# Kernel tuning notes

Hardware: AMD Instinct MI355X
Metric: run time of the kernel (lower is better)

## Reference

```python
import jax, jax.numpy as jnp
import numpy as np

D = 1024          # dim_in == dim_out
H = 16            # num_heads
G = 4             # num_kv_groups
HD = D // H       # head_dim = 64
GS = H // G       # group_size = 4
S = 2048          # context_length / seq_len
B = 2
EPS = 1e-05


def setup_inputs() -> dict:
    key = jax.random.key(0)
    ks = jax.random.split(key, 12)
    sd = 0.02
    return {
        "x":  jax.random.normal(ks[0], (B, S, D), jnp.float32),
        # torch.nn.Linear weights are stored [out_features, in_features]
        "wq": jax.random.normal(ks[1], (D, D), jnp.float32) * sd,
        "wk": jax.random.normal(ks[2], (G * HD, D), jnp.float32) * sd,
        "wv": jax.random.normal(ks[3], (G * HD, D), jnp.float32) * sd,
        "wo": jax.random.normal(ks[4], (D, D), jnp.float32) * sd,
        "w1": jax.random.normal(ks[5], (4 * D, D), jnp.float32) * sd,
        "w2": jax.random.normal(ks[6], (D, 4 * D), jnp.float32) * sd,
        "g1": jnp.ones((D,), jnp.float32),
        "b1": jnp.zeros((D,), jnp.float32),
        "g2": jnp.ones((D,), jnp.float32),
        "b2": jnp.zeros((D,), jnp.float32),
    }


def _layernorm(x, gamma, beta):
    mean = jnp.mean(x, axis=-1, keepdims=True)
    var = jnp.var(x, axis=-1, keepdims=True)  # unbiased=False
    return (x - mean) * jax.lax.rsqrt(var + EPS) * gamma + beta


def _gelu_tanh(x):
    c = jnp.sqrt(jnp.asarray(2.0 / jnp.pi, x.dtype))
    return 0.5 * x * (1.0 + jnp.tanh(c * (x + 0.044715 * x ** 3)))


def _gqa(x, wq, wk, wv, wo):
    b, s, _ = x.shape
    q = (x @ wq.T).reshape(b, s, H, HD).transpose(0, 2, 1, 3)   # [B,H,S,hd]
    k = (x @ wk.T).reshape(b, s, G, HD).transpose(0, 2, 1, 3)   # [B,G,S,hd]
    v = (x @ wv.T).reshape(b, s, G, HD).transpose(0, 2, 1, 3)
    k = jnp.repeat(k, GS, axis=1)                               # [B,H,S,hd]
    v = jnp.repeat(v, GS, axis=1)
    scores = jnp.einsum('bhqd,bhkd->bhqk', q, k)                # [B,H,S,S]
    causal = jnp.tril(jnp.ones((s, s), bool))
    scores = jnp.where(causal, scores, -jnp.inf)
    attn = jax.nn.softmax(scores / jnp.sqrt(jnp.asarray(HD, scores.dtype)), axis=-1)
    ctx = jnp.einsum('bhqk,bhkd->bhqd', attn, v)                # [B,H,S,hd]
    ctx = ctx.transpose(0, 2, 1, 3).reshape(b, s, D)
    return ctx @ wo.T


def reference(x, wq, wk, wv, wo, w1, w2, g1, b1, g2, b2):
    h = x + _gqa(_layernorm(x, g1, b1), wq, wk, wv, wo)
    ff = _layernorm(h, g2, b2) @ w1.T
    ff = _gelu_tanh(ff) @ w2.T
    return h + ff
```

## Files before the change

kernel.cpp:

```cpp
#include <hip/hip_runtime.h>
#include <stdint.h>

typedef __bf16 bf16_t;
typedef bf16_t bf16x8 __attribute__((ext_vector_type(8)));
typedef bf16_t bf16x4 __attribute__((ext_vector_type(4)));
typedef float f32x4 __attribute__((ext_vector_type(4)));

#define DEVFN static __device__ __forceinline__

DEVFN void gload_lds16(const void* g, void* l) {
  __builtin_amdgcn_global_load_lds((const __attribute__((address_space(1))) void*)g,
                                   (__attribute__((address_space(3))) void*)l, 16, 0, 0);
}

DEVFN float gelu_f(float x) {
  float u = 0.7978845608028654f * (x + 0.044715f * x * x * x);
  float e = __expf(2.0f * u);
  float t = 1.0f - 2.0f / (e + 1.0f);
  return 0.5f * x * (1.0f + t);
}

template <int CTRL>
DEVFN float dpp_rot(float x) {
  int i = __builtin_bit_cast(int, x);
  int r = __builtin_amdgcn_update_dpp(i, i, CTRL, 0xF, 0xF, false);
  return __builtin_bit_cast(float, r);
}
DEVFN float dpp_sum16(float x) {
  x += dpp_rot<0x121>(x);
  x += dpp_rot<0x122>(x);
  x += dpp_rot<0x124>(x);
  x += dpp_rot<0x128>(x);
  return x;
}

__global__ void cvt_kernel(const float* __restrict__ s, bf16_t* __restrict__ d, int n4) {
  int i = blockIdx.x * blockDim.x + threadIdx.x;
  int stride = gridDim.x * blockDim.x;
  for (; i < n4; i += stride) {
    float4 v = ((const float4*)s)[i];
    bf16x4 o;
    o[0] = (bf16_t)v.x; o[1] = (bf16_t)v.y; o[2] = (bf16_t)v.z; o[3] = (bf16_t)v.w;
    ((bf16x4*)d)[i] = o;
  }
}

__global__ __launch_bounds__(256) void ln_kernel(const float* __restrict__ in,
                                                 const float* __restrict__ gamma,
                                                 const float* __restrict__ beta,
                                                 bf16_t* __restrict__ out) {
  const int row = blockIdx.x;
  const int tid = threadIdx.x;
  const float4 v = ((const float4*)(in + (size_t)row * 1024))[tid];
  float s = v.x + v.y + v.z + v.w;
  float q = v.x * v.x + v.y * v.y + v.z * v.z + v.w * v.w;
#pragma unroll
  for (int off = 1; off < 64; off <<= 1) {
    s += __shfl_xor(s, off);
    q += __shfl_xor(q, off);
  }
  __shared__ float ss[4], qs[4];
  if ((tid & 63) == 0) { ss[tid >> 6] = s; qs[tid >> 6] = q; }
  __syncthreads();
  s = ss[0] + ss[1] + ss[2] + ss[3];
  q = qs[0] + qs[1] + qs[2] + qs[3];
  const float mean = s * (1.0f / 1024.0f);
  const float var = q * (1.0f / 1024.0f) - mean * mean;
  const float rstd = rsqrtf(var + 1e-5f);
  const float4 g4 = ((const float4*)gamma)[tid];
  const float4 b4 = ((const float4*)beta)[tid];
  bf16x4 o;
  o[0] = (bf16_t)((v.x - mean) * rstd * g4.x + b4.x);
  o[1] = (bf16_t)((v.y - mean) * rstd * g4.y + b4.y);
  o[2] = (bf16_t)((v.z - mean) * rstd * g4.z + b4.z);
  o[3] = (bf16_t)((v.w - mean) * rstd * g4.w + b4.w);
  *(bf16x4*)(out + (size_t)row * 1024 + tid * 4) = o;
}

template <int EPI, int BM>
__global__ __launch_bounds__(256, (BM == 64 ? 4 : 2))
void gemm_bt(const bf16_t* __restrict__ A, const bf16_t* __restrict__ W,
             bf16_t* outb, float* outf, const float* resid, int M, int N, int K) {
  constexpr int MI = BM / 32;
  constexpr int WRS = BM / 2;
  __shared__ __align__(16) bf16_t As[BM * 32];
  __shared__ __align__(16) bf16_t Bs[128 * 32];
  const int tid = threadIdx.x;
  const int lane = tid & 63;
  const int wid = tid >> 6;
  const int l15 = lane & 15;
  const int l4 = lane >> 4;
  const int m0 = blockIdx.y * BM;
  const int n0 = blockIdx.x * 128;
  const int wr = wid >> 1;
  const int wc = wid & 1;

  const int sr = lane >> 2;
  const int sk = (lane & 3) * 8;
  const bf16_t* aBase;
  bf16_t* aDst0;
  if constexpr (BM == 128) {
    aBase = A + (size_t)(m0 + wid * 32 + sr) * K + sk;
    aDst0 = &As[wid * 1024];
  } else {
    aBase = A + (size_t)(m0 + wid * 16 + sr) * K + sk;
    aDst0 = &As[wid * 512];
  }
  const bf16_t* bBase = W + (size_t)(n0 + wid * 32 + sr) * K + sk;
  bf16_t* bDst0 = &Bs[wid * 1024];
  const size_t rowOff16 = (size_t)16 * K;

  f32x4 acc[MI][4] = {};

  for (int kt = 0; kt < K; kt += 32) {
    gload_lds16(aBase + kt, aDst0);
    if constexpr (BM == 128) gload_lds16(aBase + kt + rowOff16, aDst0 + 512);
    gload_lds16(bBase + kt, bDst0);
    gload_lds16(bBase + kt + rowOff16, bDst0 + 512);
    __syncthreads();
    bf16x8 af[MI], bfr[4];
#pragma unroll
    for (int i = 0; i < MI; ++i)
      af[i] = *(const bf16x8*)&As[(wr * WRS + i * 16 + l15) * 32 + l4 * 8];
#pragma unroll
    for (int j = 0; j < 4; ++j)
      bfr[j] = *(const bf16x8*)&Bs[(wc * 64 + j * 16 + l15) * 32 + l4 * 8];
#pragma unroll
    for (int i = 0; i < MI; ++i)
#pragma unroll
      for (int j = 0; j < 4; ++j)
        acc[i][j] = __builtin_amdgcn_mfma_f32_16x16x32_bf16(af[i], bfr[j], acc[i][j], 0, 0, 0);
    __syncthreads();
  }

  const int col0 = n0 + wc * 64 + l15;
  const int row0 = m0 + wr * WRS + l4 * 4;
#pragma unroll
  for (int i = 0; i < MI; ++i) {
#pragma unroll
    for (int r = 0; r < 4; ++r) {
      const size_t row = (size_t)(row0 + i * 16 + r);
#pragma unroll
      for (int j = 0; j < 4; ++j) {
        const size_t idx = row * N + col0 + j * 16;
        const float v = acc[i][j][r];
        if constexpr (EPI == 0) {
          outb[idx] = (bf16_t)v;
        } else if constexpr (EPI == 1) {
          outb[idx] = (bf16_t)gelu_f(v);
        } else {
          outf[idx] = resid[idx] + v;
        }
      }
    }
  }
}

static __device__ const int kQbTab[40] = {0,1,2,3,4,4,5,5,6,6,7,7,8,8,8,9,9,9,10,10,10,
                                          11,11,11,12,12,12,12,13,13,13,13,14,14,14,14,15,15,15,15};
static __device__ const int kCTab[40]  = {0,0,0,0,0,1,0,1,0,1,0,1,0,1,2,0,1,2,0,1,2,
                                          0,1,2,0,1,2,3,0,1,2,3,0,1,2,3,0,1,2,3};
static __device__ const int kPrefix16[16] = {0,1,2,3,4,6,8,10,12,15,18,21,24,28,32,36};

__global__ __launch_bounds__(256, 3) void attn_kernel(const bf16_t* __restrict__ qkv,
                                                      bf16_t* __restrict__ pO,
                                                      float* __restrict__ pML) {
  __shared__ __align__(16) bf16_t Ks[2][64 * 68];
  __shared__ __align__(16) bf16_t Vt[2][64 * 68];
  __shared__ __align__(16) bf16_t Ps[4][32 * 68];
  const int tid = threadIdx.x, lane = tid & 63, wid = tid >> 6;
  const int l15 = lane & 15, l4 = lane >> 4;
  const int bx = blockIdx.x;
  const int qb = kQbTab[bx] * 128;
  const int kv_lo = kCTab[bx] * 512;
  const int kv_hi = min(qb + 128, kv_lo + 512);
  const int h = blockIdx.y, b = blockIdx.z;
  const int g = h >> 2;
  const int slot = (b * 16 + h) * 40 + bx;
  const size_t RS = 1536;
  const bf16_t* qbase = qkv + (size_t)b * 2048 * RS + h * 64;
  const bf16_t* kbase = qkv + (size_t)b * 2048 * RS + 1024 + g * 64;
  const bf16_t* vbase = kbase + 256;
  const float C2S = 0.125f * 1.44269504088896340736f;

  bf16x8 qf[2][2];
#pragma unroll
  for (int rf = 0; rf < 2; ++rf)
#pragma unroll
    for (int kc = 0; kc < 2; ++kc) {
      bf16x8 raw = *(const bf16x8*)(qbase + (size_t)(qb + wid * 32 + rf * 16 + l15) * RS +
                                    kc * 32 + l4 * 8);
#pragma unroll
      for (int e = 0; e < 8; ++e) qf[rf][kc][e] = (bf16_t)((float)raw[e] * C2S);
    }

  f32x4 po[2][4] = {};
  float l_i[2][4] = {};

  const int sKrow = tid >> 2, sKc = (tid & 3) * 16;
  const int sVkey = tid & 63, sVd = (tid >> 6) * 16;
  const bf16_t* kRowPtr = kbase + (size_t)sKrow * RS + sKc;
  const bf16_t* vRowPtr = vbase + (size_t)sVkey * RS + sVd;

  uint4 k0 = *(const uint4*)(kRowPtr + (size_t)kv_lo * RS);
  uint4 k1 = *(const uint4*)(kRowPtr + (size_t)kv_lo * RS + 8);
  bf16x8 v0 = *(const bf16x8*)(vRowPtr + (size_t)kv_lo * RS);
  bf16x8 v1 = *(const bf16x8*)(vRowPtr + (size_t)kv_lo * RS + 8);
  *(uint4*)&Ks[0][sKrow * 68 + sKc] = k0;
  *(uint4*)&Ks[0][sKrow * 68 + sKc + 8] = k1;
#pragma unroll
  for (int i = 0; i < 8; ++i) {
    Vt[0][(sVd + i) * 68 + sVkey] = v0[i];
    Vt[0][(sVd + 8 + i) * 68 + sVkey] = v1[i];
  }

  const int fb0 = qb + wid * 32;
  int cur = 0;
  for (int kv0 = kv_lo; kv0 < kv_hi; kv0 += 64) {
    __syncthreads();
    const bool more = (kv0 + 64) < kv_hi;
    if (more) {
      const bf16_t* kp = kRowPtr + (size_t)(kv0 + 64) * RS;
      const bf16_t* vp = vRowPtr + (size_t)(kv0 + 64) * RS;
      k0 = *(const uint4*)kp;
      k1 = *(const uint4*)(kp + 8);
      v0 = *(const bf16x8*)vp;
      v1 = *(const bf16x8*)(vp + 8);
    }

    f32x4 sAcc[2][4] = {};
#pragma unroll
    for (int jt = 0; jt < 4; ++jt) {
#pragma unroll
      for (int kc = 0; kc < 2; ++kc) {
        bf16x8 kf = *(const bf16x8*)&Ks[cur][(jt * 16 + l15) * 68 + kc * 32 + l4 * 8];
        sAcc[0][jt] = __builtin_amdgcn_mfma_f32_16x16x32_bf16(qf[0][kc], kf, sAcc[0][jt], 0, 0, 0);
        sAcc[1][jt] = __builtin_amdgcn_mfma_f32_16x16x32_bf16(qf[1][kc], kf, sAcc[1][jt], 0, 0, 0);
      }
    }

#pragma unroll
    for (int rf = 0; rf < 2; ++rf) {
      const int fb = fb0 + rf * 16;
      if (kv0 > fb + 15) continue;
      bf16_t* psb = &Ps[wid][(rf * 16 + l4 * 4) * 68 + l15];
      float rsum[4] = {0.f, 0.f, 0.f, 0.f};
      const bool diag = (kv0 + 63 > fb);
#pragma unroll
      for (int jt = 0; jt < 4; ++jt)
#pragma unroll
        for (int r = 0; r < 4; ++r) {
          float sv = sAcc[rf][jt][r];
          if (diag) {
            const int key = kv0 + jt * 16 + l15;
            sv = (key <= fb + l4 * 4 + r) ? sv : -3.0e38f;
          }
          const float e = exp2f(sv);
          rsum[r] += e;
          psb[r * 68 + jt * 16] = (bf16_t)e;
        }
#pragma unroll
      for (int r = 0; r < 4; ++r) l_i[rf][r] += dpp_sum16(rsum[r]);
    }

    if (kv0 <= fb0 + 31) {
      const bool do0 = (kv0 <= fb0 + 15);
#pragma unroll
      for (int kc = 0; kc < 2; ++kc) {
        bf16x8 pa1 = *(const bf16x8*)&Ps[wid][(16 + l15) * 68 + kc * 32 + l4 * 8];
        bf16x8 pa0;
        if (do0) pa0 = *(const bf16x8*)&Ps[wid][l15 * 68 + kc * 32 + l4 * 8];
#pragma unroll
        for (int jd = 0; jd < 4; ++jd) {
          bf16x8 vf = *(const bf16x8*)&Vt[cur][(jd * 16 + l15) * 68 + kc * 32 + l4 * 8];
          if (do0) po[0][jd] = __builtin_amdgcn_mfma_f32_16x16x32_bf16(pa0, vf, po[0][jd], 0, 0, 0);
          po[1][jd] = __builtin_amdgcn_mfma_f32_16x16x32_bf16(pa1, vf, po[1][jd], 0, 0, 0);
        }
      }
    }

    if (more) {
      *(uint4*)&Ks[cur ^ 1][sKrow * 68 + sKc] = k0;
      *(uint4*)&Ks[cur ^ 1][sKrow * 68 + sKc + 8] = k1;
#pragma unroll
      for (int i = 0; i < 8; ++i) {
        Vt[cur ^ 1][(sVd + i) * 68 + sVkey] = v0[i];
        Vt[cur ^ 1][(sVd + 8 + i) * 68 + sVkey] = v1[i];
      }
    }
    cur ^= 1;
  }

#pragma unroll
  for (int rf = 0; rf < 2; ++rf) {
#pragma unroll
    for (int r = 0; r < 4; ++r) {
      const int lrow = wid * 32 + rf * 16 + l4 * 4 + r;
      if (l15 == 0) {
        pML[((size_t)slot * 128 + lrow) * 2] = 0.0f;
        pML[((size_t)slot * 128 + lrow) * 2 + 1] = l_i[rf][r];
      }
#pragma unroll
      for (int jd = 0; jd < 4; ++jd)
        pO[((size_t)slot * 128 + lrow) * 64 + jd * 16 + l15] = (bf16_t)po[rf][jd][r];
    }
  }
}

__global__ __launch_bounds__(256) void attn_combine(const bf16_t* __restrict__ pO,
                                                    const float* __restrict__ pML,
                                                    bf16_t* __restrict__ ctx) {
  const int i = blockIdx.x, h = blockIdx.y, b = blockIdx.z;
  const int C = (i >> 2) + 1;
  const int base = (b * 16 + h) * 40 + kPrefix16[i];
  const int row = threadIdx.x >> 1;
  const int half = (threadIdx.x & 1) * 32;
  float m = -3.0e38f;
  for (int c = 0; c < C; ++c)
    m = fmaxf(m, pML[((size_t)(base + c) * 128 + row) * 2]);
  float L = 0.0f, acc[32];
#pragma unroll
  for (int e = 0; e < 32; ++e) acc[e] = 0.0f;
  for (int c = 0; c < C; ++c) {
    const float mc = pML[((size_t)(base + c) * 128 + row) * 2];
    const float lc = pML[((size_t)(base + c) * 128 + row) * 2 + 1];
    const float w = exp2f(mc - m);
    L += w * lc;
    const bf16_t* op = pO + ((size_t)(base + c) * 128 + row) * 64 + half;
#pragma unroll
    for (int j = 0; j < 4; ++j) {
      bf16x8 v = *(const bf16x8*)(op + j * 8);
#pragma unroll
      for (int e = 0; e < 8; ++e) acc[j * 8 + e] += w * (float)v[e];
    }
  }
  const float inv = 1.0f / L;
  bf16_t* outp = ctx + ((size_t)b * 2048 + i * 128 + row) * 1024 + h * 64 + half;
#pragma unroll
  for (int j = 0; j < 4; ++j) {
    bf16x8 o;
#pragma unroll
    for (int e = 0; e < 8; ++e) o[e] = (bf16_t)(acc[j * 8 + e] * inv);
    *(bf16x8*)(outp + j * 8) = o;
  }
}

extern "C" void kernel_launch(void* const* d_in, const int* in_sizes, int n_in,
                              void* d_out, int out_size, void* d_ws, size_t ws_size,
                              hipStream_t stream) {
  const float* x = (const float*)d_in[0];
  const float* wq = (const float*)d_in[1];
  const float* wk = (const float*)d_in[2];
  const float* wv = (const float*)d_in[3];
  const float* wo = (const float*)d_in[4];
  const float* w1 = (const float*)d_in[5];
  const float* w2 = (const float*)d_in[6];
  const float* g1 = (const float*)d_in[7];
  const float* b1 = (const float*)d_in[8];
  const float* g2 = (const float*)d_in[9];
  const float* b2 = (const float*)d_in[10];
  float* out = (float*)d_out;

  char* ws = (char*)d_ws;
  bf16_t* qkv = (bf16_t*)(ws + 0);
  bf16_t* ctx = (bf16_t*)(ws + 12582912);
  bf16_t* wo_b = (bf16_t*)(ws + 20971520);
  bf16_t* wqkv_b = (bf16_t*)(ws + 23068672);
  bf16_t* h1 = (bf16_t*)(ws + 26214400);
  bf16_t* pO = (bf16_t*)(ws + 23068672);
  float* pML = (float*)(ws + 45088768);
  bf16_t* w1_b = (bf16_t*)(ws + 0);
  bf16_t* w2_b = (bf16_t*)(ws + 8388608);
  bf16_t* h2 = (bf16_t*)(ws + 16777216);
  bf16_t* ff = (bf16_t*)(ws + 25165824);

  auto cvt = [&](const float* s, bf16_t* d, int n) {
    int n4 = n / 4;
    int grid = (n4 + 255) / 256;
    if (grid > 2048) grid = 2048;
    cvt_kernel<<<grid, 256, 0, stream>>>(s, d, n4);
  };
  cvt(wq, wqkv_b, 1048576);
  cvt(wk, wqkv_b + 1048576, 262144);
  cvt(wv, wqkv_b + 1310720, 262144);
  cvt(wo, wo_b, 1048576);

  ln_kernel<<<4096, 256, 0, stream>>>(x, g1, b1, h1);
  gemm_bt<0, 64><<<dim3(12, 64), 256, 0, stream>>>(h1, wqkv_b, qkv, nullptr, nullptr, 4096, 1536, 1024);
  attn_kernel<<<dim3(40, 16, 2), 256, 0, stream>>>(qkv, pO, pML);
  cvt(w1, w1_b, 4194304);
  attn_combine<<<dim3(16, 16, 2), 256, 0, stream>>>(pO, pML, ctx);
  gemm_bt<2, 64><<<dim3(8, 64), 256, 0, stream>>>(ctx, wo_b, nullptr, out, x, 4096, 1024, 1024);
  cvt(w2, w2_b, 4194304);
  ln_kernel<<<4096, 256, 0, stream>>>(out, g2, b2, h2);
  gemm_bt<1, 128><<<dim3(32, 32), 256, 0, stream>>>(h2, w1_b, ff, nullptr, nullptr, 4096, 4096, 1024);
  gemm_bt<2, 64><<<dim3(8, 64), 256, 0, stream>>>(ff, w2_b, nullptr, out, out, 4096, 1024, 4096);
}
```

Before: 270.4 us.

## Double-buffer GEMM K-loop with 64-wide stages and merge weight conversion launches

The GEMM main loop now uses two LDS buffers, each holding two 32-wide K slices. The next 64-wide K stage is issued as async global-to-LDS loads before the current stage is computed, which halves the barrier count and overlaps memory with MFMA work. The min-blocks occupancy hint for BM=64 drops from 4 to 3 to allow for the larger LDS footprint. The four separate weight-conversion launches are also merged into one kernel to cut launch overhead. One risk: there is a single barrier per iteration while the next stage writes into the other buffer. Reads of that buffer from two iterations earlier are fenced only by that one barrier, which looks correct, but the async LDS writes are not explicitly waited on (vmcnt) before the barrier.

```diff
diff --git a/kernel.cpp b/kernel.cpp
--- a/kernel.cpp
+++ b/kernel.cpp
@@ -42,6 +42,26 @@
     bf16x4 o;
     o[0] = (bf16_t)v.x; o[1] = (bf16_t)v.y; o[2] = (bf16_t)v.z; o[3] = (bf16_t)v.w;
     ((bf16x4*)d)[i] = o;
+  }
+}
+
+__global__ void cvt4_kernel(const float* __restrict__ wq, const float* __restrict__ wk,
+                            const float* __restrict__ wv, const float* __restrict__ wo,
+                            bf16_t* __restrict__ qkv_dst, bf16_t* __restrict__ wo_dst) {
+  int i = blockIdx.x * blockDim.x + threadIdx.x;
+  int stride = gridDim.x * blockDim.x;
+  for (; i < 655360; i += stride) {
+    const float* s;
+    bf16_t* d;
+    int j;
+    if (i < 262144) { s = wq; d = qkv_dst; j = i; }
+    else if (i < 327680) { s = wk; d = qkv_dst + 1048576; j = i - 262144; }
+    else if (i < 393216) { s = wv; d = qkv_dst + 1310720; j = i - 327680; }
+    else { s = wo; d = wo_dst; j = i - 393216; }
+    float4 v = ((const float4*)s)[j];
+    bf16x4 o;
+    o[0] = (bf16_t)v.x; o[1] = (bf16_t)v.y; o[2] = (bf16_t)v.z; o[3] = (bf16_t)v.w;
+    ((bf16x4*)d)[j] = o;
   }
 }
 
@@ -78,13 +98,13 @@
 }
 
 template <int EPI, int BM>
-__global__ __launch_bounds__(256, (BM == 64 ? 4 : 2))
+__global__ __launch_bounds__(256, (BM == 64 ? 3 : 2))
 void gemm_bt(const bf16_t* __restrict__ A, const bf16_t* __restrict__ W,
              bf16_t* outb, float* outf, const float* resid, int M, int N, int K) {
   constexpr int MI = BM / 32;
   constexpr int WRS = BM / 2;
-  __shared__ __align__(16) bf16_t As[BM * 32];
-  __shared__ __align__(16) bf16_t Bs[128 * 32];
+  __shared__ __align__(16) bf16_t As[2][2][BM * 32];
+  __shared__ __align__(16) bf16_t Bs[2][2][128 * 32];
   const int tid = threadIdx.x;
   const int lane = tid & 63;
   const int wid = tid >> 6;
@@ -98,39 +118,50 @@
   const int sr = lane >> 2;
   const int sk = (lane & 3) * 8;
   const bf16_t* aBase;
-  bf16_t* aDst0;
-  if constexpr (BM == 128) {
-    aBase = A + (size_t)(m0 + wid * 32 + sr) * K + sk;
-    aDst0 = &As[wid * 1024];
-  } else {
-    aBase = A + (size_t)(m0 + wid * 16 + sr) * K + sk;
-    aDst0 = &As[wid * 512];
-  }
+  if constexpr (BM == 128) aBase = A + (size_t)(m0 + wid * 32 + sr) * K + sk;
+  else                     aBase = A + (size_t)(m0 + wid * 16 + sr) * K + sk;
   const bf16_t* bBase = W + (size_t)(n0 + wid * 32 + sr) * K + sk;
-  bf16_t* bDst0 = &Bs[wid * 1024];
   const size_t rowOff16 = (size_t)16 * K;
 
   f32x4 acc[MI][4] = {};
-
-  for (int kt = 0; kt < K; kt += 32) {
-    gload_lds16(aBase + kt, aDst0);
-    if constexpr (BM == 128) gload_lds16(aBase + kt + rowOff16, aDst0 + 512);
-    gload_lds16(bBase + kt, bDst0);
-    gload_lds16(bBase + kt + rowOff16, bDst0 + 512);
+  const int NT = K / 64;
+
+  auto stage = [&](int buf, int t) {
+    const int kt = t * 64;
+#pragma unroll
+    for (int kk = 0; kk < 2; ++kk) {
+      const int ko = kt + kk * 32;
+      if constexpr (BM == 128) {
+        gload_lds16(aBase + ko, &As[buf][kk][wid * 1024]);
+        gload_lds16(aBase + ko + rowOff16, &As[buf][kk][wid * 1024 + 512]);
+      } else {
+        gload_lds16(aBase + ko, &As[buf][kk][wid * 512]);
+      }
+      gload_lds16(bBase + ko, &Bs[buf][kk][wid * 1024]);
+      gload_lds16(bBase + ko + rowOff16, &Bs[buf][kk][wid * 1024 + 512]);
+    }
+  };
+
+  stage(0, 0);
+  for (int t = 0; t < NT; ++t) {
     __syncthreads();
-    bf16x8 af[MI], bfr[4];
-#pragma unroll
-    for (int i = 0; i < MI; ++i)
-      af[i] = *(const bf16x8*)&As[(wr * WRS + i * 16 + l15) * 32 + l4 * 8];
-#pragma unroll
-    for (int j = 0; j < 4; ++j)
-      bfr[j] = *(const bf16x8*)&Bs[(wc * 64 + j * 16 + l15) * 32 + l4 * 8];
-#pragma unroll
-    for (int i = 0; i < MI; ++i)
+    if (t + 1 < NT) stage((t + 1) & 1, t + 1);
+    const int buf = t & 1;
+#pragma unroll
+    for (int kk = 0; kk < 2; ++kk) {
+      bf16x8 af[MI], bfr[4];
+#pragma unroll
+      for (int i = 0; i < MI; ++i)
+        af[i] = *(const bf16x8*)&As[buf][kk][(wr * WRS + i * 16 + l15) * 32 + l4 * 8];
 #pragma unroll
       for (int j = 0; j < 4; ++j)
-        acc[i][j] = __builtin_amdgcn_mfma_f32_16x16x32_bf16(af[i], bfr[j], acc[i][j], 0, 0, 0);
-    __syncthreads();
+        bfr[j] = *(const bf16x8*)&Bs[buf][kk][(wc * 64 + j * 16 + l15) * 32 + l4 * 8];
+#pragma unroll
+      for (int i = 0; i < MI; ++i)
+#pragma unroll
+        for (int j = 0; j < 4; ++j)
+          acc[i][j] = __builtin_amdgcn_mfma_f32_16x16x32_bf16(af[i], bfr[j], acc[i][j], 0, 0, 0);
+    }
   }
 
   const int col0 = n0 + wc * 64 + l15;
@@ -380,10 +411,7 @@
     if (grid > 2048) grid = 2048;
     cvt_kernel<<<grid, 256, 0, stream>>>(s, d, n4);
   };
-  cvt(wq, wqkv_b, 1048576);
-  cvt(wk, wqkv_b + 1048576, 262144);
-  cvt(wv, wqkv_b + 1310720, 262144);
-  cvt(wo, wo_b, 1048576);
+  cvt4_kernel<<<2048, 256, 0, stream>>>(wq, wk, wv, wo, wqkv_b, wo_b);
 
   ln_kernel<<<4096, 256, 0, stream>>>(x, g1, b1, h1);
   gemm_bt<0, 64><<<dim3(12, 64), 256, 0, stream>>>(h1, wqkv_b, qkv, nullptr, nullptr, 4096, 1536, 1024);
```

After: 257.5 us. 4.8% less time.
